# Kernel optimization log

Hardware: AMD Instinct MI355X
Metric: run time of the kernel (lower is better)

The kernel has to match this reference:

```python
import jax, jax.numpy as jnp
import numpy as np

NUM_HEADS = 16
D_K = 64  # d_model // num_heads = 1024 // 16


def setup_inputs() -> dict:
    key = jax.random.key(0)
    ks = jax.random.split(key, 5)
    b, s, d = 2, 2048, 1024
    scale = 0.02
    return {
        "x": jax.random.normal(ks[0], (b, s, d), dtype=jnp.float32),
        "W_qkv": jax.random.normal(ks[1], (d, 3 * d), dtype=jnp.float32) * scale,
        "b_qkv": jax.random.normal(ks[2], (3 * d,), dtype=jnp.float32) * scale,
        "W_o": jax.random.normal(ks[3], (d, d), dtype=jnp.float32) * scale,
        "b_o": jax.random.normal(ks[4], (d,), dtype=jnp.float32) * scale,
    }


def reference(x, W_qkv, b_qkv, W_o, b_o):
    b, s, d = x.shape
    h, dk = NUM_HEADS, D_K
    # fused QKV projection: (b, s, 3*d_model)
    qkv = x @ W_qkv + b_qkv
    # faithful to the torch rearrange 'b s (h d)' with d = 3*d_k, then chunk:
    # each head's contiguous 3*d_k slice is split into q, k, v.
    qkv = qkv.reshape(b, s, h, 3 * dk).transpose(0, 2, 1, 3)  # (b, h, s, 3*dk)
    q, k, v = jnp.split(qkv, 3, axis=-1)  # each (b, h, s, dk)
    inv_scale = 1.0 / np.float32(np.sqrt(dk))
    scores = jnp.einsum("bhqd,bhkd->bhqk", q, k) * inv_scale  # (b, h, s, s)
    attn = jax.nn.softmax(scores, axis=-1)
    ctx = jnp.einsum("bhqk,bhkd->bhqd", attn, v)  # (b, h, s, dk)
    ctx = ctx.transpose(0, 2, 1, 3).reshape(b, s, d)  # (b, s, d_model)
    return ctx @ W_o + b_o
```

## Files before the change

### kernel.cpp

```cpp
#include <hip/hip_runtime.h>
#include <hip/hip_bf16.h>
#include <stdint.h>

#define NHEADS 16
#define DKH    64
#define BB     2
#define SS     2048
#define DM     1024
#define MROWS  (BB * SS)

typedef __attribute__((ext_vector_type(8))) short bf8_t;
typedef __attribute__((ext_vector_type(4))) float f4_t;
typedef unsigned short u16;
typedef uint32_t u32;

__device__ __forceinline__ u16 f2bf(float f) {
    union { float f; u32 u; } v; v.f = f;
    return (u16)((v.u + 0x7fffu + ((v.u >> 16) & 1u)) >> 16);
}

__device__ __forceinline__ u32 cvt_pk_bf16(float lo, float hi) {
    u32 r;
    asm("v_cvt_pk_bf16_f32 %0, %1, %2" : "=v"(r) : "v"(lo), "v"(hi));
    return r;
}

__device__ __forceinline__ float fexp2(float x) {
#if __has_builtin(__builtin_amdgcn_exp2f)
    return __builtin_amdgcn_exp2f(x);
#else
    return __expf(x * 0.69314718056f);
#endif
}

__device__ __forceinline__ void async_copy16(void* lds, const void* g) {
    __builtin_amdgcn_global_load_lds(
        (__attribute__((address_space(1))) void*)(void*)g,
        (__attribute__((address_space(3))) void*)lds, 16, 0, 0);
}

#define MFMA32(a, b, c) __builtin_amdgcn_mfma_f32_16x16x32_bf16(a, b, c, 0, 0, 0)

__global__ void k_cvt(const float* __restrict__ in, u16* __restrict__ out, int n4) {
    int stride = gridDim.x * blockDim.x;
    for (int i = blockIdx.x * blockDim.x + threadIdx.x; i < n4; i += stride) {
        float4 v = ((const float4*)in)[i];
        ushort4 o;
        o.x = f2bf(v.x); o.y = f2bf(v.y); o.z = f2bf(v.z); o.w = f2bf(v.w);
        ((ushort4*)out)[i] = o;
    }
}

__global__ void k_transpose(const float* __restrict__ W, u16* __restrict__ Wt, int K, int N) {
    __shared__ float tile[32][33];
    int n0 = blockIdx.x * 32, k0 = blockIdx.y * 32;
    int tx = threadIdx.x & 31, ty = threadIdx.x >> 5;
    #pragma unroll
    for (int r = ty; r < 32; r += 8)
        tile[r][tx] = W[(size_t)(k0 + r) * N + n0 + tx];
    __syncthreads();
    #pragma unroll
    for (int r = ty; r < 32; r += 8)
        Wt[(size_t)(n0 + r) * K + k0 + tx] = f2bf(tile[tx][r]);
}

__global__ __launch_bounds__(256) void k_vt(const u16* __restrict__ V, u16* __restrict__ Vt) {
    __shared__ u16 t[64][72];
    const int bh = blockIdx.y;
    const int s0 = blockIdx.x * 64;
    const u16* Vb = V + (size_t)bh * SS * DKH;
    u16* Tb = Vt + (size_t)bh * DKH * SS;
    const int tid = threadIdx.x;
    #pragma unroll
    for (int it = 0; it < 2; ++it) {
        const int c = tid + it * 256;
        const int r = c >> 3, sl = c & 7;
        *(uint4*)&t[r][sl * 8] = *(const uint4*)(Vb + (size_t)(s0 + r) * DKH + sl * 8);
    }
    __syncthreads();
    #pragma unroll
    for (int it = 0; it < 2; ++it) {
        const int c = tid + it * 256;
        const int d = c >> 3, sl = c & 7;
        uint4 o;
        o.x = t[sl * 8 + 0][d] | ((u32)t[sl * 8 + 1][d] << 16);
        o.y = t[sl * 8 + 2][d] | ((u32)t[sl * 8 + 3][d] << 16);
        o.z = t[sl * 8 + 4][d] | ((u32)t[sl * 8 + 5][d] << 16);
        o.w = t[sl * 8 + 6][d] | ((u32)t[sl * 8 + 7][d] << 16);
        *(uint4*)(Tb + (size_t)d * SS + s0 + sl * 8) = o;
    }
}

template<int MODE, int BMT, int BNT>
__global__ __launch_bounds__(256) void k_gemm(
    const u16* __restrict__ A, const u16* __restrict__ Bt,
    const float* __restrict__ bias,
    u16* __restrict__ q_out, u16* __restrict__ k_out, u16* __restrict__ v_out,
    float* __restrict__ f_out,
    int N, int K)
{
    constexpr int MF = BMT / 32, NF = BNT / 32;
    __shared__ u16 As[BMT * 32];
    __shared__ u16 Bs[BNT * 32];
    const int m0 = blockIdx.y * BMT, n0 = blockIdx.x * BNT;
    const int tid = threadIdx.x;
    const int w = tid >> 6, l = tid & 63;
    const int lr = l >> 2, lc = (l & 3) * 8;
    const int fr = l & 15, fk = (l >> 4) * 8;
    const int wm = (w >> 1) * (BMT / 2), wn = (w & 1) * (BNT / 2);
    f4_t acc[MF][NF] = {};

    for (int kt = 0; kt < K; kt += 32) {
        #pragma unroll
        for (int c = w; c < BMT / 16; c += 4)
            async_copy16(As + c * 512, A  + (size_t)(m0 + c * 16 + lr) * K + kt + lc);
        #pragma unroll
        for (int c = w; c < BNT / 16; c += 4)
            async_copy16(Bs + c * 512, Bt + (size_t)(n0 + c * 16 + lr) * K + kt + lc);
        __syncthreads();
        bf8_t af[MF], bfr[NF];
        #pragma unroll
        for (int mf = 0; mf < MF; ++mf)
            af[mf] = *(const bf8_t*)&As[(wm + mf * 16 + fr) * 32 + fk];
        #pragma unroll
        for (int nf = 0; nf < NF; ++nf)
            bfr[nf] = *(const bf8_t*)&Bs[(wn + nf * 16 + fr) * 32 + fk];
        #pragma unroll
        for (int mf = 0; mf < MF; ++mf)
            #pragma unroll
            for (int nf = 0; nf < NF; ++nf)
                acc[mf][nf] = MFMA32(af[mf], bfr[nf], acc[mf][nf]);
        __syncthreads();
    }

    #pragma unroll
    for (int mf = 0; mf < MF; ++mf)
      #pragma unroll
      for (int nf = 0; nf < NF; ++nf)
        #pragma unroll
        for (int j = 0; j < 4; ++j) {
            const int m = m0 + wm + mf * 16 + (l >> 4) * 4 + j;
            const int n = n0 + wn + nf * 16 + (l & 15);
            float v = acc[mf][nf][j] + bias[n];
            if (MODE == 0) {
                const int h = n / 192, rem = n - h * 192;
                const int which = rem >> 6, dd = rem & 63;
                const int b = m >> 11, s = m & (SS - 1);
                const size_t idx = ((size_t)(b * NHEADS + h) * SS + s) * DKH + dd;
                u16* dst = (which == 0) ? q_out : ((which == 1) ? k_out : v_out);
                dst[idx] = f2bf(v);
            } else {
                f_out[(size_t)m * N + n] = v;
            }
        }
}

#define SCL 0.180336880f

__global__ __launch_bounds__(256, 4) void k_attn(
    const u16* __restrict__ Qg, const u16* __restrict__ Kg, const u16* __restrict__ Vtg,
    u16* __restrict__ ctx)
{
    __shared__ u16 Ks[128 * 64];
    __shared__ u16 Vs[64 * 128];
    const int bh = blockIdx.x;
    const int qt = blockIdx.y;
    const int tid = threadIdx.x, w = tid >> 6, l = tid & 63;
    const int fr = l & 15, fq = l >> 4;
    const int q0 = qt * 64 + w * 16;
    const u16* Qb = Qg  + (size_t)bh * SS * DKH;
    const u16* Kb = Kg  + (size_t)bh * SS * DKH;
    const u16* Vb = Vtg + (size_t)bh * DKH * SS;

    bf8_t qf[2];
    #pragma unroll
    for (int kh = 0; kh < 2; ++kh)
        qf[kh] = *(const bf8_t*)(Qb + (size_t)(q0 + fr) * DKH + kh * 32 + fq * 8);

    float mrow = -__builtin_inff(), lrow = 0.f;
    f4_t o[4] = {};

    for (int kv = 0; kv < SS; kv += 128) {
        #pragma unroll
        for (int it = 0; it < 4; ++it) {
            const int c = tid + it * 256;
            const int cb = it * 256 + w * 64;
            const int rk = c >> 3;
            const int slk = (c & 7) ^ (rk & 7);
            const int sr = ((rk >> 2) & 3) * 32 + (rk >> 4) * 4 + (rk & 3);
            async_copy16(Ks + cb * 8, Kb + (size_t)(kv + sr) * DKH + slk * 8);
            const int rv = c >> 4;
            const int slv = (c & 15) ^ (rv & 7);
            async_copy16(Vs + cb * 8, Vb + (size_t)rv * SS + kv + slv * 8);
        }
        __syncthreads();

        f4_t sa[8] = {};
        #pragma unroll
        for (int nf = 0; nf < 8; ++nf)
          #pragma unroll
          for (int kh = 0; kh < 2; ++kh) {
            const int row = nf * 16 + fr;
            const int dsl = (kh * 4 + fq) ^ (fr & 7);
            const bf8_t kb = *(const bf8_t*)&Ks[row * 64 + dsl * 8];
            sa[nf] = MFMA32(kb, qf[kh], sa[nf]);
          }

        float x = sa[0][0];
        #pragma unroll
        for (int nf = 0; nf < 8; ++nf)
          #pragma unroll
          for (int j = 0; j < 4; ++j)
            x = fmaxf(x, sa[nf][j]);
        x *= SCL;
        x = fmaxf(x, __shfl_xor(x, 16));
        x = fmaxf(x, __shfl_xor(x, 32));

        if (__any(x > mrow + 8.f)) {
            float mnew = fmaxf(mrow, x);
            float sc = fexp2(mrow - mnew);
            lrow *= sc;
            mrow = mnew;
            float sc4[4];
            #pragma unroll
            for (int j = 0; j < 4; ++j) sc4[j] = __shfl(sc, fq * 4 + j);
            #pragma unroll
            for (int df = 0; df < 4; ++df)
              #pragma unroll
              for (int j = 0; j < 4; ++j)
                o[df][j] *= sc4[j];
        }

        float ps = 0.f;
        u32 pk[16];
        #pragma unroll
        for (int nf = 0; nf < 8; ++nf) {
            float p0 = fexp2(sa[nf][0] * SCL - mrow);
            float p1 = fexp2(sa[nf][1] * SCL - mrow);
            float p2 = fexp2(sa[nf][2] * SCL - mrow);
            float p3 = fexp2(sa[nf][3] * SCL - mrow);
            ps += (p0 + p1) + (p2 + p3);
            pk[nf * 2 + 0] = cvt_pk_bf16(p0, p1);
            pk[nf * 2 + 1] = cvt_pk_bf16(p2, p3);
        }
        ps += __shfl_xor(ps, 16);
        ps += __shfl_xor(ps, 32);
        lrow += ps;

        #pragma unroll
        for (int t = 0; t < 4; ++t) {
            union { bf8_t v; u32 u[4]; } pa;
            pa.u[0] = pk[4 * t + 0]; pa.u[1] = pk[4 * t + 1];
            pa.u[2] = pk[4 * t + 2]; pa.u[3] = pk[4 * t + 3];
            const int sl = fq * 4 + t;
            #pragma unroll
            for (int df = 0; df < 4; ++df) {
                const int rv = df * 16 + fr;
                const int dsl = sl ^ (rv & 7);
                const bf8_t vv = *(const bf8_t*)&Vs[rv * 128 + dsl * 8];
                o[df] = MFMA32(pa.v, vv, o[df]);
            }
        }
        __syncthreads();
    }

    float ml[4];
    #pragma unroll
    for (int j = 0; j < 4; ++j) ml[j] = __shfl(lrow, fq * 4 + j);

    const int b = bh >> 4, h = bh & 15;
    #pragma unroll
    for (int df = 0; df < 4; ++df)
      #pragma unroll
      for (int j = 0; j < 4; ++j) {
        const int s = q0 + fq * 4 + j;
        const int dd = df * 16 + fr;
        float v = o[df][j] / ml[j];
        ctx[((size_t)(b * SS + s)) * DM + h * DKH + dd] = f2bf(v);
      }
}

extern "C" void kernel_launch(void* const* d_in, const int* in_sizes, int n_in,
                              void* d_out, int out_size, void* d_ws, size_t ws_size,
                              hipStream_t stream)
{
    const float* x     = (const float*)d_in[0];
    const float* W_qkv = (const float*)d_in[1];
    const float* b_qkv = (const float*)d_in[2];
    const float* W_o   = (const float*)d_in[3];
    const float* b_o   = (const float*)d_in[4];
    float* out = (float*)d_out;

    char* ws = (char*)d_ws;
    u16* xb   = (u16*)(ws);
    u16* Wqkt = (u16*)(ws + 8388608);
    u16* Wot  = (u16*)(ws + 8388608 + 6291456);
    u16* Qg   = (u16*)(ws + 16777216);
    u16* Kg   = Qg  + 4194304;
    u16* Vg   = Kg  + 4194304;
    u16* Vtg  = Vg  + 4194304;
    u16* ctx  = xb;

    k_cvt<<<1024, 256, 0, stream>>>(x, xb, (MROWS * DM) / 4);
    k_transpose<<<dim3(3 * DM / 32, DM / 32), 256, 0, stream>>>(W_qkv, Wqkt, DM, 3 * DM);
    k_transpose<<<dim3(DM / 32, DM / 32), 256, 0, stream>>>(W_o, Wot, DM, DM);
    k_gemm<0, 128, 128><<<dim3(3 * DM / 128, MROWS / 128), 256, 0, stream>>>(
        xb, Wqkt, b_qkv, Qg, Kg, Vg, nullptr, 3 * DM, DM);
    k_vt<<<dim3(SS / 64, BB * NHEADS), 256, 0, stream>>>(Vg, Vtg);
    k_attn<<<dim3(BB * NHEADS, SS / 64), 256, 0, stream>>>(Qg, Kg, Vtg, ctx);
    k_gemm<1, 64, 64><<<dim3(DM / 64, MROWS / 64), 256, 0, stream>>>(
        ctx, Wot, b_o, nullptr, nullptr, nullptr, out, DM, DM);
}
```

Baseline: 198.1 us.

## Double-buffer GEMM and attention loads, widen attention q-tile, merge prep kernels

```diff
diff --git a/kernel.cpp b/kernel.cpp
--- a/kernel.cpp
+++ b/kernel.cpp
@@ -41,27 +41,43 @@
 
 #define MFMA32(a, b, c) __builtin_amdgcn_mfma_f32_16x16x32_bf16(a, b, c, 0, 0, 0)
 
-__global__ void k_cvt(const float* __restrict__ in, u16* __restrict__ out, int n4) {
-    int stride = gridDim.x * blockDim.x;
-    for (int i = blockIdx.x * blockDim.x + threadIdx.x; i < n4; i += stride) {
-        float4 v = ((const float4*)in)[i];
-        ushort4 o;
-        o.x = f2bf(v.x); o.y = f2bf(v.y); o.z = f2bf(v.z); o.w = f2bf(v.w);
-        ((ushort4*)out)[i] = o;
-    }
-}
-
-__global__ void k_transpose(const float* __restrict__ W, u16* __restrict__ Wt, int K, int N) {
+__global__ __launch_bounds__(256) void k_prep(
+    const float* __restrict__ x, const float* __restrict__ Wqkv,
+    const float* __restrict__ Wo,
+    u16* __restrict__ xb, u16* __restrict__ Wqkt, u16* __restrict__ Wot)
+{
     __shared__ float tile[32][33];
-    int n0 = blockIdx.x * 32, k0 = blockIdx.y * 32;
-    int tx = threadIdx.x & 31, ty = threadIdx.x >> 5;
-    #pragma unroll
-    for (int r = ty; r < 32; r += 8)
-        tile[r][tx] = W[(size_t)(k0 + r) * N + n0 + tx];
-    __syncthreads();
-    #pragma unroll
-    for (int r = ty; r < 32; r += 8)
-        Wt[(size_t)(n0 + r) * K + k0 + tx] = f2bf(tile[tx][r]);
+    const int blk = blockIdx.x;
+    const int tx = threadIdx.x & 31, ty = threadIdx.x >> 5;
+    if (blk < 3072) {
+        const int n0 = (blk % 96) * 32, k0 = (blk / 96) * 32;
+        #pragma unroll
+        for (int r = ty; r < 32; r += 8)
+            tile[r][tx] = Wqkv[(size_t)(k0 + r) * (3 * DM) + n0 + tx];
+        __syncthreads();
+        #pragma unroll
+        for (int r = ty; r < 32; r += 8)
+            Wqkt[(size_t)(n0 + r) * DM + k0 + tx] = f2bf(tile[tx][r]);
+    } else if (blk < 4096) {
+        const int b2 = blk - 3072;
+        const int n0 = (b2 % 32) * 32, k0 = (b2 / 32) * 32;
+        #pragma unroll
+        for (int r = ty; r < 32; r += 8)
+            tile[r][tx] = Wo[(size_t)(k0 + r) * DM + n0 + tx];
+        __syncthreads();
+        #pragma unroll
+        for (int r = ty; r < 32; r += 8)
+            Wot[(size_t)(n0 + r) * DM + k0 + tx] = f2bf(tile[tx][r]);
+    } else {
+        const int b2 = blk - 4096;
+        const int n4 = (MROWS * DM) / 4;
+        for (int i = b2 * 256 + threadIdx.x; i < n4; i += 512 * 256) {
+            float4 v = ((const float4*)x)[i];
+            ushort4 o;
+            o.x = f2bf(v.x); o.y = f2bf(v.y); o.z = f2bf(v.z); o.w = f2bf(v.w);
+            ((ushort4*)xb)[i] = o;
+        }
+    }
 }
 
 __global__ __launch_bounds__(256) void k_vt(const u16* __restrict__ V, u16* __restrict__ Vt) {
@@ -100,8 +116,8 @@
     int N, int K)
 {
     constexpr int MF = BMT / 32, NF = BNT / 32;
-    __shared__ u16 As[BMT * 32];
-    __shared__ u16 Bs[BNT * 32];
+    __shared__ u16 As[2][BMT * 32];
+    __shared__ u16 Bs[2][BNT * 32];
     const int m0 = blockIdx.y * BMT, n0 = blockIdx.x * BNT;
     const int tid = threadIdx.x;
     const int w = tid >> 6, l = tid & 63;
@@ -110,27 +126,38 @@
     const int wm = (w >> 1) * (BMT / 2), wn = (w & 1) * (BNT / 2);
     f4_t acc[MF][NF] = {};
 
+    auto stage = [&](int kt, int buf) {
+        #pragma unroll
+        for (int cc = 0; cc < BMT / 64; ++cc) {
+            const int c = w + cc * 4;
+            async_copy16(&As[buf][c * 512], A + (size_t)(m0 + c * 16 + lr) * K + kt + lc);
+        }
+        #pragma unroll
+        for (int cc = 0; cc < BNT / 64; ++cc) {
+            const int c = w + cc * 4;
+            async_copy16(&Bs[buf][c * 512], Bt + (size_t)(n0 + c * 16 + lr) * K + kt + lc);
+        }
+    };
+
+    stage(0, 0);
+    __syncthreads();
+    int cur = 0;
     for (int kt = 0; kt < K; kt += 32) {
-        #pragma unroll
-        for (int c = w; c < BMT / 16; c += 4)
-            async_copy16(As + c * 512, A  + (size_t)(m0 + c * 16 + lr) * K + kt + lc);
-        #pragma unroll
-        for (int c = w; c < BNT / 16; c += 4)
-            async_copy16(Bs + c * 512, Bt + (size_t)(n0 + c * 16 + lr) * K + kt + lc);
-        __syncthreads();
+        if (kt + 32 < K) stage(kt + 32, cur ^ 1);
         bf8_t af[MF], bfr[NF];
         #pragma unroll
         for (int mf = 0; mf < MF; ++mf)
-            af[mf] = *(const bf8_t*)&As[(wm + mf * 16 + fr) * 32 + fk];
+            af[mf] = *(const bf8_t*)&As[cur][(wm + mf * 16 + fr) * 32 + fk];
         #pragma unroll
         for (int nf = 0; nf < NF; ++nf)
-            bfr[nf] = *(const bf8_t*)&Bs[(wn + nf * 16 + fr) * 32 + fk];
+            bfr[nf] = *(const bf8_t*)&Bs[cur][(wn + nf * 16 + fr) * 32 + fk];
         #pragma unroll
         for (int mf = 0; mf < MF; ++mf)
             #pragma unroll
             for (int nf = 0; nf < NF; ++nf)
                 acc[mf][nf] = MFMA32(af[mf], bfr[nf], acc[mf][nf]);
         __syncthreads();
+        cur ^= 1;
     }
 
     #pragma unroll
@@ -157,30 +184,33 @@
 
 #define SCL 0.180336880f
 
-__global__ __launch_bounds__(256, 4) void k_attn(
+__global__ __launch_bounds__(256, 2) void k_attn(
     const u16* __restrict__ Qg, const u16* __restrict__ Kg, const u16* __restrict__ Vtg,
     u16* __restrict__ ctx)
 {
-    __shared__ u16 Ks[128 * 64];
-    __shared__ u16 Vs[64 * 128];
+    __shared__ u16 Ks[2][128 * 64];
+    __shared__ u16 Vs[2][64 * 128];
     const int bh = blockIdx.x;
     const int qt = blockIdx.y;
     const int tid = threadIdx.x, w = tid >> 6, l = tid & 63;
     const int fr = l & 15, fq = l >> 4;
-    const int q0 = qt * 64 + w * 16;
+    const int q0 = qt * 128 + w * 32;
     const u16* Qb = Qg  + (size_t)bh * SS * DKH;
     const u16* Kb = Kg  + (size_t)bh * SS * DKH;
     const u16* Vb = Vtg + (size_t)bh * DKH * SS;
 
-    bf8_t qf[2];
-    #pragma unroll
-    for (int kh = 0; kh < 2; ++kh)
-        qf[kh] = *(const bf8_t*)(Qb + (size_t)(q0 + fr) * DKH + kh * 32 + fq * 8);
-
-    float mrow = -__builtin_inff(), lrow = 0.f;
-    f4_t o[4] = {};
-
-    for (int kv = 0; kv < SS; kv += 128) {
+    bf8_t qf[2][2];
+    #pragma unroll
+    for (int mf = 0; mf < 2; ++mf)
+      #pragma unroll
+      for (int kh = 0; kh < 2; ++kh)
+        qf[mf][kh] = *(const bf8_t*)(Qb + (size_t)(q0 + mf * 16 + fr) * DKH + kh * 32 + fq * 8);
+
+    float mrow[2] = {-__builtin_inff(), -__builtin_inff()};
+    float lrow[2] = {0.f, 0.f};
+    f4_t o[2][4] = {};
+
+    auto stage = [&](int kv, int buf) {
         #pragma unroll
         for (int it = 0; it < 4; ++it) {
             const int c = tid + it * 256;
@@ -188,96 +218,109 @@
             const int rk = c >> 3;
             const int slk = (c & 7) ^ (rk & 7);
             const int sr = ((rk >> 2) & 3) * 32 + (rk >> 4) * 4 + (rk & 3);
-            async_copy16(Ks + cb * 8, Kb + (size_t)(kv + sr) * DKH + slk * 8);
+            async_copy16(&Ks[buf][cb * 8], Kb + (size_t)(kv + sr) * DKH + slk * 8);
             const int rv = c >> 4;
             const int slv = (c & 15) ^ (rv & 7);
-            async_copy16(Vs + cb * 8, Vb + (size_t)rv * SS + kv + slv * 8);
-        }
-        __syncthreads();
-
-        f4_t sa[8] = {};
-        #pragma unroll
-        for (int nf = 0; nf < 8; ++nf)
-          #pragma unroll
-          for (int kh = 0; kh < 2; ++kh) {
-            const int row = nf * 16 + fr;
-            const int dsl = (kh * 4 + fq) ^ (fr & 7);
-            const bf8_t kb = *(const bf8_t*)&Ks[row * 64 + dsl * 8];
-            sa[nf] = MFMA32(kb, qf[kh], sa[nf]);
-          }
-
-        float x = sa[0][0];
-        #pragma unroll
-        for (int nf = 0; nf < 8; ++nf)
-          #pragma unroll
-          for (int j = 0; j < 4; ++j)
-            x = fmaxf(x, sa[nf][j]);
-        x *= SCL;
-        x = fmaxf(x, __shfl_xor(x, 16));
-        x = fmaxf(x, __shfl_xor(x, 32));
-
-        if (__any(x > mrow + 8.f)) {
-            float mnew = fmaxf(mrow, x);
-            float sc = fexp2(mrow - mnew);
-            lrow *= sc;
-            mrow = mnew;
-            float sc4[4];
-            #pragma unroll
-            for (int j = 0; j < 4; ++j) sc4[j] = __shfl(sc, fq * 4 + j);
-            #pragma unroll
-            for (int df = 0; df < 4; ++df)
+            async_copy16(&Vs[buf][cb * 8], Vb + (size_t)rv * SS + kv + slv * 8);
+        }
+    };
+
+    stage(0, 0);
+    __syncthreads();
+    int cur = 0;
+    for (int kv = 0; kv < SS; kv += 128) {
+        if (kv + 128 < SS) stage(kv + 128, cur ^ 1);
+
+        u32 pk[2][16];
+        #pragma unroll
+        for (int mf = 0; mf < 2; ++mf) {
+            f4_t sa[8] = {};
+            #pragma unroll
+            for (int nf = 0; nf < 8; ++nf)
+              #pragma unroll
+              for (int kh = 0; kh < 2; ++kh) {
+                const int row = nf * 16 + fr;
+                const int dsl = (kh * 4 + fq) ^ (fr & 7);
+                const bf8_t kb = *(const bf8_t*)&Ks[cur][row * 64 + dsl * 8];
+                sa[nf] = MFMA32(kb, qf[mf][kh], sa[nf]);
+              }
+
+            float x = sa[0][0];
+            #pragma unroll
+            for (int nf = 0; nf < 8; ++nf)
               #pragma unroll
               for (int j = 0; j < 4; ++j)
-                o[df][j] *= sc4[j];
-        }
-
-        float ps = 0.f;
-        u32 pk[16];
-        #pragma unroll
-        for (int nf = 0; nf < 8; ++nf) {
-            float p0 = fexp2(sa[nf][0] * SCL - mrow);
-            float p1 = fexp2(sa[nf][1] * SCL - mrow);
-            float p2 = fexp2(sa[nf][2] * SCL - mrow);
-            float p3 = fexp2(sa[nf][3] * SCL - mrow);
-            ps += (p0 + p1) + (p2 + p3);
-            pk[nf * 2 + 0] = cvt_pk_bf16(p0, p1);
-            pk[nf * 2 + 1] = cvt_pk_bf16(p2, p3);
-        }
-        ps += __shfl_xor(ps, 16);
-        ps += __shfl_xor(ps, 32);
-        lrow += ps;
+                x = fmaxf(x, sa[nf][j]);
+            x *= SCL;
+            x = fmaxf(x, __shfl_xor(x, 16));
+            x = fmaxf(x, __shfl_xor(x, 32));
+
+            if (__any(x > mrow[mf] + 8.f)) {
+                float mnew = fmaxf(mrow[mf], x);
+                float sc = fexp2(mrow[mf] - mnew);
+                lrow[mf] *= sc;
+                mrow[mf] = mnew;
+                float sc4[4];
+                #pragma unroll
+                for (int j = 0; j < 4; ++j) sc4[j] = __shfl(sc, fq * 4 + j);
+                #pragma unroll
+                for (int df = 0; df < 4; ++df)
+                  #pragma unroll
+                  for (int j = 0; j < 4; ++j)
+                    o[mf][df][j] *= sc4[j];
+            }
+
+            float ps = 0.f;
+            #pragma unroll
+            for (int nf = 0; nf < 8; ++nf) {
+                float p0 = fexp2(sa[nf][0] * SCL - mrow[mf]);
+                float p1 = fexp2(sa[nf][1] * SCL - mrow[mf]);
+                float p2 = fexp2(sa[nf][2] * SCL - mrow[mf]);
+                float p3 = fexp2(sa[nf][3] * SCL - mrow[mf]);
+                ps += (p0 + p1) + (p2 + p3);
+                pk[mf][nf * 2 + 0] = cvt_pk_bf16(p0, p1);
+                pk[mf][nf * 2 + 1] = cvt_pk_bf16(p2, p3);
+            }
+            ps += __shfl_xor(ps, 16);
+            ps += __shfl_xor(ps, 32);
+            lrow[mf] += ps;
+        }
 
         #pragma unroll
         for (int t = 0; t < 4; ++t) {
-            union { bf8_t v; u32 u[4]; } pa;
-            pa.u[0] = pk[4 * t + 0]; pa.u[1] = pk[4 * t + 1];
-            pa.u[2] = pk[4 * t + 2]; pa.u[3] = pk[4 * t + 3];
+            union { bf8_t v; u32 u[4]; } pa0, pa1;
+            #pragma unroll
+            for (int i = 0; i < 4; ++i) { pa0.u[i] = pk[0][4 * t + i]; pa1.u[i] = pk[1][4 * t + i]; }
             const int sl = fq * 4 + t;
             #pragma unroll
             for (int df = 0; df < 4; ++df) {
                 const int rv = df * 16 + fr;
                 const int dsl = sl ^ (rv & 7);
-                const bf8_t vv = *(const bf8_t*)&Vs[rv * 128 + dsl * 8];
-                o[df] = MFMA32(pa.v, vv, o[df]);
+                const bf8_t vv = *(const bf8_t*)&Vs[cur][rv * 128 + dsl * 8];
+                o[0][df] = MFMA32(pa0.v, vv, o[0][df]);
+                o[1][df] = MFMA32(pa1.v, vv, o[1][df]);
             }
         }
         __syncthreads();
-    }
-
-    float ml[4];
-    #pragma unroll
-    for (int j = 0; j < 4; ++j) ml[j] = __shfl(lrow, fq * 4 + j);
+        cur ^= 1;
+    }
 
     const int b = bh >> 4, h = bh & 15;
     #pragma unroll
-    for (int df = 0; df < 4; ++df)
-      #pragma unroll
-      for (int j = 0; j < 4; ++j) {
-        const int s = q0 + fq * 4 + j;
-        const int dd = df * 16 + fr;
-        float v = o[df][j] / ml[j];
-        ctx[((size_t)(b * SS + s)) * DM + h * DKH + dd] = f2bf(v);
-      }
+    for (int mf = 0; mf < 2; ++mf) {
+        float ml[4];
+        #pragma unroll
+        for (int j = 0; j < 4; ++j) ml[j] = __shfl(lrow[mf], fq * 4 + j);
+        #pragma unroll
+        for (int df = 0; df < 4; ++df)
+          #pragma unroll
+          for (int j = 0; j < 4; ++j) {
+            const int s = q0 + mf * 16 + fq * 4 + j;
+            const int dd = df * 16 + fr;
+            float v = o[mf][df][j] / ml[j];
+            ctx[((size_t)(b * SS + s)) * DM + h * DKH + dd] = f2bf(v);
+          }
+    }
 }
 
 extern "C" void kernel_launch(void* const* d_in, const int* in_sizes, int n_in,
@@ -301,13 +344,11 @@
     u16* Vtg  = Vg  + 4194304;
     u16* ctx  = xb;
 
-    k_cvt<<<1024, 256, 0, stream>>>(x, xb, (MROWS * DM) / 4);
-    k_transpose<<<dim3(3 * DM / 32, DM / 32), 256, 0, stream>>>(W_qkv, Wqkt, DM, 3 * DM);
-    k_transpose<<<dim3(DM / 32, DM / 32), 256, 0, stream>>>(W_o, Wot, DM, DM);
+    k_prep<<<4608, 256, 0, stream>>>(x, W_qkv, W_o, xb, Wqkt, Wot);
     k_gemm<0, 128, 128><<<dim3(3 * DM / 128, MROWS / 128), 256, 0, stream>>>(
         xb, Wqkt, b_qkv, Qg, Kg, Vg, nullptr, 3 * DM, DM);
     k_vt<<<dim3(SS / 64, BB * NHEADS), 256, 0, stream>>>(Vg, Vtg);
-    k_attn<<<dim3(BB * NHEADS, SS / 64), 256, 0, stream>>>(Qg, Kg, Vtg, ctx);
+    k_attn<<<dim3(BB * NHEADS, SS / 128), 256, 0, stream>>>(Qg, Kg, Vtg, ctx);
     k_gemm<1, 64, 64><<<dim3(DM / 64, MROWS / 64), 256, 0, stream>>>(
         ctx, Wot, b_o, nullptr, nullptr, nullptr, out, DM, DM);
 }
```

Result: faster. 189.6 us (-4.3%).
